# Performance work log

Measured on AMD Instinct MI355X. Metric: run time of the kernel, lower is better.

The kernel has to match this reference:

```python
import jax, jax.numpy as jnp
import numpy as np

B, N, E, H = 32, 512, 256, 8
HD = E // H
EPS = 1e-5

def setup_inputs() -> dict:
    key = jax.random.key(0)
    ks = jax.random.split(key, 10)
    x = jax.random.normal(ks[0], (B, N, E), dtype=jnp.float32)
    # boolean masks: True = masked out. Keep diagonal unmasked so no row is fully masked.
    pre = jax.random.bernoulli(ks[1], 0.1, (B, H, N, N))
    eye = jnp.eye(N, dtype=bool)
    pre_mask = jnp.where(eye[None, None, :, :], False, pre)
    post_attn_mask = jax.random.bernoulli(ks[2], 0.1, (B, N))
    s = 1.0 / np.sqrt(E)
    in_proj_w = jax.random.uniform(ks[3], (3 * E, E), jnp.float32, -s, s)
    in_proj_b = jnp.zeros((3 * E,), jnp.float32)
    out_w = jax.random.uniform(ks[4], (E, E), jnp.float32, -s, s)
    out_b = jnp.zeros((E,), jnp.float32)
    gamma = jnp.ones((E,), jnp.float32)
    beta = jnp.zeros((E,), jnp.float32)
    return {"x": x, "pre_mask": pre_mask, "post_attn_mask": post_attn_mask,
            "in_proj_w": in_proj_w, "in_proj_b": in_proj_b,
            "out_w": out_w, "out_b": out_b, "gamma": gamma, "beta": beta}

def reference(x, pre_mask, post_attn_mask, in_proj_w, in_proj_b, out_w, out_b, gamma, beta):
    b, n, e = x.shape
    # fused qkv projection (matches nn.MultiheadAttention in_proj)
    qkv = x @ in_proj_w.T + in_proj_b            # [B,N,3E]
    q, k, v = jnp.split(qkv, 3, axis=-1)
    def heads(t):
        return t.reshape(b, n, H, HD).transpose(0, 2, 1, 3)  # [B,H,N,HD]
    q, k, v = heads(q), heads(k), heads(v)
    scores = jnp.einsum('bhqd,bhkd->bhqk', q * (HD ** -0.5), k)  # [B,H,N,N]
    scores = jnp.where(pre_mask, -1e9, scores)
    w = jax.nn.softmax(scores, axis=-1)                          # [B,H,N,N]
    o = jnp.einsum('bhqk,bhkd->bhqd', w, v)                      # [B,H,N,HD]
    o = o.transpose(0, 2, 1, 3).reshape(b, n, e)
    o = o @ out_w.T + out_b
    # post-attention mask: zero outputs of unavailable agents
    o = jnp.where(post_attn_mask[:, :, None], 0.0, o)
    # residual + LayerNorm
    y = x + o
    mu = y.mean(axis=-1, keepdims=True)
    var = y.var(axis=-1, keepdims=True)
    out = (y - mu) * jax.lax.rsqrt(var + EPS) * gamma + beta
    # attn_weights averaged over heads (PyTorch default average_attn_weights=True)
    attn_weights = w.mean(axis=1)                                # [B,N,N]
    return (out, attn_weights)
```

## Files before the change

### kernel.cpp

```cpp
#include <hip/hip_runtime.h>

#define BB 32
#define NN 512
#define EE 256
#define HH 8
#define HDD 32

typedef __attribute__((ext_vector_type(4))) float f32x4;
typedef __attribute__((ext_vector_type(8))) short s16x8;
typedef unsigned short ushort_t;
typedef unsigned int uint_t;

__device__ __forceinline__ ushort_t f2bf(float f) {
  union { float f; uint_t u; } v; v.f = f;
  uint_t r = v.u + 0x7fffu + ((v.u >> 16) & 1u);
  return (ushort_t)(r >> 16);
}
__device__ __forceinline__ uint_t pk2(float a, float b) {
  return (uint_t)f2bf(a) | ((uint_t)f2bf(b) << 16);
}

__global__ __launch_bounds__(256) void cvt_bf16(
    const float* __restrict__ src, ushort_t* __restrict__ dst, int n4) {
  int i = blockIdx.x * 256 + threadIdx.x;
  if (i < n4) {
    float4 v = ((const float4*)src)[i];
    uint2 p; p.x = pk2(v.x, v.y); p.y = pk2(v.z, v.w);
    ((uint2*)dst)[i] = p;
  }
}

__global__ __launch_bounds__(256) void qkv_mfma(
    const ushort_t* __restrict__ xb, const ushort_t* __restrict__ wb,
    const float* __restrict__ bias,
    ushort_t* __restrict__ Q, ushort_t* __restrict__ K, ushort_t* __restrict__ Vt) {
  __shared__ ushort_t sA[128][40];
  __shared__ ushort_t sB[128][40];
  int t = threadIdx.x;
  int bj = blockIdx.x % 6, bm = blockIdx.x / 6;
  int m0 = bm * 128, j0 = bj * 128;
  int w4 = t >> 6, lane = t & 63, quad = lane >> 4, l16 = lane & 15;
  int wy = w4 >> 1, wx = w4 & 1;
  f32x4 acc[4][4];
  #pragma unroll
  for (int a = 0; a < 4; a++)
    #pragma unroll
    for (int b = 0; b < 4; b++) acc[a][b] = (f32x4){0.f, 0.f, 0.f, 0.f};
  int sr2 = t >> 2, sc2 = (t & 3) * 8;
  for (int kk = 0; kk < 256; kk += 32) {
    __syncthreads();
    #pragma unroll
    for (int p = 0; p < 2; p++) {
      int r = sr2 + 64 * p;
      *(s16x8*)&sA[r][sc2] = *(const s16x8*)&xb[(size_t)(m0 + r) * 256 + kk + sc2];
      *(s16x8*)&sB[r][sc2] = *(const s16x8*)&wb[(size_t)(j0 + r) * 256 + kk + sc2];
    }
    __syncthreads();
    s16x8 af[4], bf[4];
    #pragma unroll
    for (int mt = 0; mt < 4; mt++)
      af[mt] = *(const s16x8*)&sA[wy * 64 + mt * 16 + l16][quad * 8];
    #pragma unroll
    for (int jt = 0; jt < 4; jt++)
      bf[jt] = *(const s16x8*)&sB[wx * 64 + jt * 16 + l16][quad * 8];
    #pragma unroll
    for (int mt = 0; mt < 4; mt++)
      #pragma unroll
      for (int jt = 0; jt < 4; jt++)
        acc[mt][jt] = __builtin_amdgcn_mfma_f32_16x16x32_bf16(af[mt], bf[jt], acc[mt][jt], 0, 0, 0);
  }
  #pragma unroll
  for (int jt = 0; jt < 4; jt++) {
    int j = j0 + wx * 64 + jt * 16 + l16;
    int which = j >> 8, e0 = j & 255, h = e0 >> 5, d0 = e0 & 31;
    float b = bias[j];
    #pragma unroll
    for (int mt = 0; mt < 4; mt++) {
      #pragma unroll
      for (int r = 0; r < 4; r++) {
        int m = m0 + wy * 64 + mt * 16 + quad * 4 + r;
        int bi = m >> 9, n = m & 511;
        ushort_t val = f2bf(acc[mt][jt][r] + b);
        if (which == 2) {
          Vt[((size_t)(bi * 8 + h) * 32 + d0) * 512 + n] = val;
        } else {
          ushort_t* dst = (which == 0) ? Q : K;
          dst[((size_t)(bi * 8 + h) * 512 + n) * 32 + d0] = val;
        }
      }
    }
  }
}

__global__ __launch_bounds__(256) void attn_kernel(
    const ushort_t* __restrict__ Q, const ushort_t* __restrict__ K,
    const ushort_t* __restrict__ Vt, const int* __restrict__ pre_mask,
    ushort_t* __restrict__ O, float* __restrict__ attnw) {
  __shared__ ushort_t sQ[16 * 32];
  __shared__ ushort_t sP[16 * 520];
  __shared__ float sSum[4][16];
  __shared__ float sO[4][16 * 32];

  int t = threadIdx.x;
  int bb = blockIdx.x >> 5;
  int q0 = (blockIdx.x & 31) << 4;
  int w = t >> 6;
  int lane = t & 63;
  int quad = lane >> 4;
  int l16 = lane & 15;
  int kbase = w * 128;
  const float scale = 0.17677669529663687f;

  float wmean[4][8];
  #pragma unroll
  for (int i = 0; i < 4; i++)
    #pragma unroll
    for (int j = 0; j < 8; j++) wmean[i][j] = 0.f;

  for (int h = 0; h < 8; h++) {
    size_t base = ((size_t)(bb * 8 + h) * 512) * 32;
    const ushort_t* Kg = K + base;
    const ushort_t* Vg = Vt + base;
    const int* mbase = pre_mask + ((size_t)(bb * 8 + h) * 512 + q0) * 512;

    if (t < 64) {
      ((s16x8*)sQ)[t] = ((const s16x8*)(Q + base + (size_t)q0 * 32))[t];
    }
    __syncthreads();

    s16x8 afrag = *(const s16x8*)&sQ[l16 * 32 + quad * 8];
    float ev[8][4];
    #pragma unroll
    for (int t8 = 0; t8 < 8; t8++) {
      int n0 = kbase + t8 * 16;
      s16x8 bfrag = *(const s16x8*)&Kg[(size_t)(n0 + l16) * 32 + quad * 8];
      f32x4 acc = {0.f, 0.f, 0.f, 0.f};
      acc = __builtin_amdgcn_mfma_f32_16x16x32_bf16(afrag, bfrag, acc, 0, 0, 0);
      #pragma unroll
      for (int i = 0; i < 4; i++) {
        int msk = mbase[(quad * 4 + i) * 512 + n0 + l16];
        ev[t8][i] = msk ? 0.f : __expf(acc[i] * scale);
      }
    }
    float ps[4];
    #pragma unroll
    for (int i = 0; i < 4; i++) {
      float s = 0.f;
      #pragma unroll
      for (int t8 = 0; t8 < 8; t8++) s += ev[t8][i];
      s += __shfl_xor(s, 1, 64);
      s += __shfl_xor(s, 2, 64);
      s += __shfl_xor(s, 4, 64);
      s += __shfl_xor(s, 8, 64);
      ps[i] = s;
    }
    if (l16 == 0) {
      #pragma unroll
      for (int i = 0; i < 4; i++) sSum[w][quad * 4 + i] = ps[i];
    }
    #pragma unroll
    for (int t8 = 0; t8 < 8; t8++)
      #pragma unroll
      for (int i = 0; i < 4; i++)
        sP[(quad * 4 + i) * 520 + kbase + t8 * 16 + l16] = f2bf(ev[t8][i]);
    __syncthreads();

    float inv[4];
    #pragma unroll
    for (int i = 0; i < 4; i++) {
      int r = quad * 4 + i;
      inv[i] = 1.0f / (sSum[0][r] + sSum[1][r] + sSum[2][r] + sSum[3][r]);
    }
    #pragma unroll
    for (int t8 = 0; t8 < 8; t8++)
      #pragma unroll
      for (int i = 0; i < 4; i++)
        wmean[i][t8] += 0.125f * ev[t8][i] * inv[i];

    f32x4 oacc[2];
    oacc[0] = (f32x4){0.f, 0.f, 0.f, 0.f};
    oacc[1] = (f32x4){0.f, 0.f, 0.f, 0.f};
    #pragma unroll
    for (int ks = 0; ks < 4; ks++) {
      s16x8 pa = *(const s16x8*)&sP[l16 * 520 + kbase + ks * 32 + quad * 8];
      #pragma unroll
      for (int dt = 0; dt < 2; dt++) {
        s16x8 vb = *(const s16x8*)&Vg[(size_t)(dt * 16 + l16) * 512 + kbase + ks * 32 + quad * 8];
        oacc[dt] = __builtin_amdgcn_mfma_f32_16x16x32_bf16(pa, vb, oacc[dt], 0, 0, 0);
      }
    }
    #pragma unroll
    for (int dt = 0; dt < 2; dt++)
      #pragma unroll
      for (int i = 0; i < 4; i++)
        sO[w][(quad * 4 + i) * 32 + dt * 16 + l16] = oacc[dt][i];
    __syncthreads();

    {
      int r = t >> 4;
      int c = (t & 15) * 2;
      float s0 = sO[0][r * 32 + c] + sO[1][r * 32 + c] + sO[2][r * 32 + c] + sO[3][r * 32 + c];
      float s1 = sO[0][r * 32 + c + 1] + sO[1][r * 32 + c + 1] + sO[2][r * 32 + c + 1] + sO[3][r * 32 + c + 1];
      float invr = 1.0f / (sSum[0][r] + sSum[1][r] + sSum[2][r] + sSum[3][r]);
      uint_t pk = pk2(s0 * invr, s1 * invr);
      *(uint_t*)&O[((size_t)(bb * 512 + q0 + r) * 256) + h * 32 + c] = pk;
    }
  }

  float* arow = attnw + (size_t)(bb * 512 + q0) * 512;
  #pragma unroll
  for (int i = 0; i < 4; i++)
    #pragma unroll
    for (int t8 = 0; t8 < 8; t8++)
      arow[(quad * 4 + i) * 512 + kbase + t8 * 16 + l16] = wmean[i][t8];
}

__global__ __launch_bounds__(256) void proj_ln_mfma(
    const ushort_t* __restrict__ O, const float* __restrict__ x,
    const ushort_t* __restrict__ wb, const float* __restrict__ bias,
    const int* __restrict__ post_mask,
    const float* __restrict__ gamma, const float* __restrict__ beta,
    float* __restrict__ out) {
  __shared__ ushort_t sB[256][40];
  int t = threadIdx.x;
  int m0 = blockIdx.x * 64;
  int w4 = t >> 6, lane = t & 63, quad = lane >> 4, l16 = lane & 15;
  int mrow0 = m0 + w4 * 16;
  f32x4 acc[16];
  #pragma unroll
  for (int jt = 0; jt < 16; jt++) acc[jt] = (f32x4){0.f, 0.f, 0.f, 0.f};
  int sr2 = t >> 2, sc2 = (t & 3) * 8;
  for (int kk = 0; kk < 256; kk += 32) {
    __syncthreads();
    #pragma unroll
    for (int p = 0; p < 4; p++) {
      int r = sr2 + 64 * p;
      *(s16x8*)&sB[r][sc2] = *(const s16x8*)&wb[(size_t)r * 256 + kk + sc2];
    }
    __syncthreads();
    s16x8 af = *(const s16x8*)&O[(size_t)(mrow0 + l16) * 256 + kk + quad * 8];
    #pragma unroll
    for (int jt = 0; jt < 16; jt++) {
      s16x8 bf = *(const s16x8*)&sB[jt * 16 + l16][quad * 8];
      acc[jt] = __builtin_amdgcn_mfma_f32_16x16x32_bf16(af, bf, acc[jt], 0, 0, 0);
    }
  }
  #pragma unroll
  for (int i = 0; i < 4; i++) {
    int m = mrow0 + quad * 4 + i;
    int bi = m >> 9, n = m & 511;
    bool msk = post_mask[bi * 512 + n] != 0;
    float y[16];
    float s1 = 0.f, s2 = 0.f;
    #pragma unroll
    for (int jt = 0; jt < 16; jt++) {
      int j = jt * 16 + l16;
      float p = msk ? 0.f : (acc[jt][i] + bias[j]);
      float yy = x[(size_t)m * 256 + j] + p;
      y[jt] = yy; s1 += yy; s2 += yy * yy;
    }
    s1 += __shfl_xor(s1, 1, 64); s1 += __shfl_xor(s1, 2, 64);
    s1 += __shfl_xor(s1, 4, 64); s1 += __shfl_xor(s1, 8, 64);
    s2 += __shfl_xor(s2, 1, 64); s2 += __shfl_xor(s2, 2, 64);
    s2 += __shfl_xor(s2, 4, 64); s2 += __shfl_xor(s2, 8, 64);
    float mu = s1 * (1.0f / 256.0f);
    float var = s2 * (1.0f / 256.0f) - mu * mu;
    float rstd = rsqrtf(var + 1e-5f);
    #pragma unroll
    for (int jt = 0; jt < 16; jt++) {
      int j = jt * 16 + l16;
      out[(size_t)m * 256 + j] = (y[jt] - mu) * rstd * gamma[j] + beta[j];
    }
  }
}

extern "C" void kernel_launch(void* const* d_in, const int* in_sizes, int n_in,
                              void* d_out, int out_size, void* d_ws, size_t ws_size,
                              hipStream_t stream) {
  const float* x       = (const float*)d_in[0];
  const int*   pre_m   = (const int*)d_in[1];
  const int*   post_m  = (const int*)d_in[2];
  const float* in_w    = (const float*)d_in[3];
  const float* in_b    = (const float*)d_in[4];
  const float* out_w   = (const float*)d_in[5];
  const float* out_b   = (const float*)d_in[6];
  const float* gamma   = (const float*)d_in[7];
  const float* beta    = (const float*)d_in[8];
  float* out   = (float*)d_out;
  float* attnw = out + (size_t)BB * NN * EE;
  ushort_t* Q  = (ushort_t*)d_ws;
  ushort_t* K  = Q  + (size_t)BB * HH * NN * HDD;
  ushort_t* Vt = K  + (size_t)BB * HH * NN * HDD;
  ushort_t* O  = Vt + (size_t)BB * HH * NN * HDD;
  ushort_t* xb  = O  + (size_t)BB * NN * EE;
  ushort_t* wib = xb + (size_t)BB * NN * EE;
  ushort_t* wob = wib + (size_t)3 * EE * EE;

  cvt_bf16<<<dim3(4096), dim3(256), 0, stream>>>(x, xb, BB * NN * EE / 4);
  cvt_bf16<<<dim3(192), dim3(256), 0, stream>>>(in_w, wib, 3 * EE * EE / 4);
  cvt_bf16<<<dim3(64), dim3(256), 0, stream>>>(out_w, wob, EE * EE / 4);
  qkv_mfma<<<dim3(768), dim3(256), 0, stream>>>(xb, wib, in_b, Q, K, Vt);
  attn_kernel<<<dim3(1024), dim3(256), 0, stream>>>(Q, K, Vt, pre_m, O, attnw);
  proj_ln_mfma<<<dim3(256), dim3(256), 0, stream>>>(O, x, wob, out_b, post_m, gamma, beta, out);
}
```

Baseline: 486.4 us.

## Fuse output projection and LayerNorm into attention kernel; merge conversion launches

Folds the output projection GEMM, residual add, post-mask and LayerNorm into the attention kernel. Each block keeps its 16-row bf16 head outputs in shared memory and multiplies them by out_w read straight from global memory, so the O round trip through global memory and one launch go away. The three bf16 conversion kernels become a single launch. Softmax probabilities now go to per-wave shared tiles in place of a register array, the softmax-sum buffer is double-buffered by head parity, and the head average is read back from the bf16 tiles. That lowers register pressure but computes the averaged weights from rounded values, and each block re-reads the full out_w matrix.

Result: faster. 456.5 us (-6.2%).

```diff
diff --git a/kernel.cpp b/kernel.cpp
--- a/kernel.cpp
+++ b/kernel.cpp
@@ -19,15 +19,26 @@
 __device__ __forceinline__ uint_t pk2(float a, float b) {
   return (uint_t)f2bf(a) | ((uint_t)f2bf(b) << 16);
 }
-
-__global__ __launch_bounds__(256) void cvt_bf16(
-    const float* __restrict__ src, ushort_t* __restrict__ dst, int n4) {
+__device__ __forceinline__ float bf2f(ushort_t u) {
+  union { uint_t u; float f; } v; v.u = ((uint_t)u) << 16;
+  return v.f;
+}
+
+__global__ __launch_bounds__(256) void cvt_all(
+    const float* __restrict__ x, const float* __restrict__ w1, const float* __restrict__ w2,
+    ushort_t* __restrict__ xb, ushort_t* __restrict__ w1b, ushort_t* __restrict__ w2b) {
+  const int NX = BB * NN * EE / 4;
+  const int NW1 = 3 * EE * EE / 4;
+  const int NW2 = EE * EE / 4;
   int i = blockIdx.x * 256 + threadIdx.x;
-  if (i < n4) {
-    float4 v = ((const float4*)src)[i];
-    uint2 p; p.x = pk2(v.x, v.y); p.y = pk2(v.z, v.w);
-    ((uint2*)dst)[i] = p;
-  }
+  const float* src; ushort_t* dst; int j;
+  if (i < NX) { src = x; dst = xb; j = i; }
+  else if (i < NX + NW1) { src = w1; dst = w1b; j = i - NX; }
+  else if (i < NX + NW1 + NW2) { src = w2; dst = w2b; j = i - NX - NW1; }
+  else return;
+  float4 v = ((const float4*)src)[j];
+  uint2 p; p.x = pk2(v.x, v.y); p.y = pk2(v.z, v.w);
+  ((uint2*)dst)[j] = p;
 }
 
 __global__ __launch_bounds__(256) void qkv_mfma(
@@ -92,24 +103,27 @@
   }
 }
 
-__global__ __launch_bounds__(256) void attn_kernel(
+__global__ __launch_bounds__(256) void attn_fused(
     const ushort_t* __restrict__ Q, const ushort_t* __restrict__ K,
     const ushort_t* __restrict__ Vt, const int* __restrict__ pre_mask,
-    ushort_t* __restrict__ O, float* __restrict__ attnw) {
-  __shared__ ushort_t sQ[16 * 32];
-  __shared__ ushort_t sP[16 * 520];
-  __shared__ float sSum[4][16];
-  __shared__ float sO[4][16 * 32];
+    const ushort_t* __restrict__ wob, const float* __restrict__ x,
+    const float* __restrict__ out_b, const int* __restrict__ post_mask,
+    const float* __restrict__ gamma, const float* __restrict__ beta,
+    float* __restrict__ out, float* __restrict__ attnw) {
+  __shared__ ushort_t sP[4][16 * 132];
+  __shared__ float sSum[2][4][16];
+  __shared__ float sO[4][16 * 33];
+  __shared__ ushort_t sO16[16 * 260];
+  __shared__ float sRed1[16][4];
+  __shared__ float sRed2[16][4];
 
   int t = threadIdx.x;
   int bb = blockIdx.x >> 5;
   int q0 = (blockIdx.x & 31) << 4;
-  int w = t >> 6;
-  int lane = t & 63;
-  int quad = lane >> 4;
-  int l16 = lane & 15;
+  int w = t >> 6, lane = t & 63, quad = lane >> 4, l16 = lane & 15;
   int kbase = w * 128;
   const float scale = 0.17677669529663687f;
+  ushort_t* mysP = &sP[w][0];
 
   float wmean[4][8];
   #pragma unroll
@@ -119,73 +133,61 @@
 
   for (int h = 0; h < 8; h++) {
     size_t base = ((size_t)(bb * 8 + h) * 512) * 32;
-    const ushort_t* Kg = K + base;
-    const ushort_t* Vg = Vt + base;
     const int* mbase = pre_mask + ((size_t)(bb * 8 + h) * 512 + q0) * 512;
 
-    if (t < 64) {
-      ((s16x8*)sQ)[t] = ((const s16x8*)(Q + base + (size_t)q0 * 32))[t];
-    }
-    __syncthreads();
-
-    s16x8 afrag = *(const s16x8*)&sQ[l16 * 32 + quad * 8];
-    float ev[8][4];
+    s16x8 afrag = *(const s16x8*)&Q[base + (size_t)(q0 + l16) * 32 + quad * 8];
+
+    float psum[4] = {0.f, 0.f, 0.f, 0.f};
     #pragma unroll
     for (int t8 = 0; t8 < 8; t8++) {
       int n0 = kbase + t8 * 16;
-      s16x8 bfrag = *(const s16x8*)&Kg[(size_t)(n0 + l16) * 32 + quad * 8];
+      s16x8 bfrag = *(const s16x8*)&K[base + (size_t)(n0 + l16) * 32 + quad * 8];
       f32x4 acc = {0.f, 0.f, 0.f, 0.f};
       acc = __builtin_amdgcn_mfma_f32_16x16x32_bf16(afrag, bfrag, acc, 0, 0, 0);
       #pragma unroll
       for (int i = 0; i < 4; i++) {
         int msk = mbase[(quad * 4 + i) * 512 + n0 + l16];
-        ev[t8][i] = msk ? 0.f : __expf(acc[i] * scale);
+        float e = msk ? 0.f : __expf(acc[i] * scale);
+        mysP[(quad * 4 + i) * 132 + t8 * 16 + l16] = f2bf(e);
+        psum[i] += e;
       }
     }
-    float ps[4];
     #pragma unroll
     for (int i = 0; i < 4; i++) {
-      float s = 0.f;
-      #pragma unroll
-      for (int t8 = 0; t8 < 8; t8++) s += ev[t8][i];
+      float s = psum[i];
       s += __shfl_xor(s, 1, 64);
       s += __shfl_xor(s, 2, 64);
       s += __shfl_xor(s, 4, 64);
       s += __shfl_xor(s, 8, 64);
-      ps[i] = s;
+      psum[i] = s;
     }
     if (l16 == 0) {
       #pragma unroll
-      for (int i = 0; i < 4; i++) sSum[w][quad * 4 + i] = ps[i];
-    }
-    #pragma unroll
-    for (int t8 = 0; t8 < 8; t8++)
-      #pragma unroll
-      for (int i = 0; i < 4; i++)
-        sP[(quad * 4 + i) * 520 + kbase + t8 * 16 + l16] = f2bf(ev[t8][i]);
+      for (int i = 0; i < 4; i++) sSum[h & 1][w][quad * 4 + i] = psum[i];
+    }
     __syncthreads();
 
     float inv[4];
     #pragma unroll
     for (int i = 0; i < 4; i++) {
       int r = quad * 4 + i;
-      inv[i] = 1.0f / (sSum[0][r] + sSum[1][r] + sSum[2][r] + sSum[3][r]);
+      inv[i] = 0.125f / (sSum[h & 1][0][r] + sSum[h & 1][1][r] + sSum[h & 1][2][r] + sSum[h & 1][3][r]);
     }
     #pragma unroll
     for (int t8 = 0; t8 < 8; t8++)
       #pragma unroll
       for (int i = 0; i < 4; i++)
-        wmean[i][t8] += 0.125f * ev[t8][i] * inv[i];
+        wmean[i][t8] += inv[i] * bf2f(mysP[(quad * 4 + i) * 132 + t8 * 16 + l16]);
 
     f32x4 oacc[2];
     oacc[0] = (f32x4){0.f, 0.f, 0.f, 0.f};
     oacc[1] = (f32x4){0.f, 0.f, 0.f, 0.f};
     #pragma unroll
     for (int ks = 0; ks < 4; ks++) {
-      s16x8 pa = *(const s16x8*)&sP[l16 * 520 + kbase + ks * 32 + quad * 8];
+      s16x8 pa = *(const s16x8*)&mysP[l16 * 132 + ks * 32 + quad * 8];
       #pragma unroll
       for (int dt = 0; dt < 2; dt++) {
-        s16x8 vb = *(const s16x8*)&Vg[(size_t)(dt * 16 + l16) * 512 + kbase + ks * 32 + quad * 8];
+        s16x8 vb = *(const s16x8*)&Vt[base + (size_t)(dt * 16 + l16) * 512 + kbase + ks * 32 + quad * 8];
         oacc[dt] = __builtin_amdgcn_mfma_f32_16x16x32_bf16(pa, vb, oacc[dt], 0, 0, 0);
       }
     }
@@ -193,83 +195,83 @@
     for (int dt = 0; dt < 2; dt++)
       #pragma unroll
       for (int i = 0; i < 4; i++)
-        sO[w][(quad * 4 + i) * 32 + dt * 16 + l16] = oacc[dt][i];
+        sO[w][(quad * 4 + i) * 33 + dt * 16 + l16] = oacc[dt][i];
     __syncthreads();
 
     {
       int r = t >> 4;
       int c = (t & 15) * 2;
-      float s0 = sO[0][r * 32 + c] + sO[1][r * 32 + c] + sO[2][r * 32 + c] + sO[3][r * 32 + c];
-      float s1 = sO[0][r * 32 + c + 1] + sO[1][r * 32 + c + 1] + sO[2][r * 32 + c + 1] + sO[3][r * 32 + c + 1];
-      float invr = 1.0f / (sSum[0][r] + sSum[1][r] + sSum[2][r] + sSum[3][r]);
-      uint_t pk = pk2(s0 * invr, s1 * invr);
-      *(uint_t*)&O[((size_t)(bb * 512 + q0 + r) * 256) + h * 32 + c] = pk;
-    }
-  }
-
-  float* arow = attnw + (size_t)(bb * 512 + q0) * 512;
-  #pragma unroll
-  for (int i = 0; i < 4; i++)
-    #pragma unroll
-    for (int t8 = 0; t8 < 8; t8++)
-      arow[(quad * 4 + i) * 512 + kbase + t8 * 16 + l16] = wmean[i][t8];
-}
-
-__global__ __launch_bounds__(256) void proj_ln_mfma(
-    const ushort_t* __restrict__ O, const float* __restrict__ x,
-    const ushort_t* __restrict__ wb, const float* __restrict__ bias,
-    const int* __restrict__ post_mask,
-    const float* __restrict__ gamma, const float* __restrict__ beta,
-    float* __restrict__ out) {
-  __shared__ ushort_t sB[256][40];
-  int t = threadIdx.x;
-  int m0 = blockIdx.x * 64;
-  int w4 = t >> 6, lane = t & 63, quad = lane >> 4, l16 = lane & 15;
-  int mrow0 = m0 + w4 * 16;
-  f32x4 acc[16];
-  #pragma unroll
-  for (int jt = 0; jt < 16; jt++) acc[jt] = (f32x4){0.f, 0.f, 0.f, 0.f};
-  int sr2 = t >> 2, sc2 = (t & 3) * 8;
-  for (int kk = 0; kk < 256; kk += 32) {
-    __syncthreads();
-    #pragma unroll
-    for (int p = 0; p < 4; p++) {
-      int r = sr2 + 64 * p;
-      *(s16x8*)&sB[r][sc2] = *(const s16x8*)&wb[(size_t)r * 256 + kk + sc2];
-    }
-    __syncthreads();
-    s16x8 af = *(const s16x8*)&O[(size_t)(mrow0 + l16) * 256 + kk + quad * 8];
-    #pragma unroll
-    for (int jt = 0; jt < 16; jt++) {
-      s16x8 bf = *(const s16x8*)&sB[jt * 16 + l16][quad * 8];
-      acc[jt] = __builtin_amdgcn_mfma_f32_16x16x32_bf16(af, bf, acc[jt], 0, 0, 0);
-    }
-  }
+      float s0 = sO[0][r * 33 + c] + sO[1][r * 33 + c] + sO[2][r * 33 + c] + sO[3][r * 33 + c];
+      float s1 = sO[0][r * 33 + c + 1] + sO[1][r * 33 + c + 1] + sO[2][r * 33 + c + 1] + sO[3][r * 33 + c + 1];
+      float invr = 1.0f / (sSum[h & 1][0][r] + sSum[h & 1][1][r] + sSum[h & 1][2][r] + sSum[h & 1][3][r]);
+      *(uint_t*)&sO16[r * 260 + h * 32 + c] = pk2(s0 * invr, s1 * invr);
+    }
+  }
+
+  {
+    float* arow = attnw + (size_t)(bb * 512 + q0) * 512;
+    #pragma unroll
+    for (int i = 0; i < 4; i++)
+      #pragma unroll
+      for (int t8 = 0; t8 < 8; t8++)
+        arow[(quad * 4 + i) * 512 + kbase + t8 * 16 + l16] = wmean[i][t8];
+  }
+  __syncthreads();
+
+  int jr0 = w * 64;
+  f32x4 pacc[4];
+  #pragma unroll
+  for (int jt = 0; jt < 4; jt++) pacc[jt] = (f32x4){0.f, 0.f, 0.f, 0.f};
+  #pragma unroll
+  for (int kc = 0; kc < 8; kc++) {
+    s16x8 pa = *(const s16x8*)&sO16[l16 * 260 + kc * 32 + quad * 8];
+    #pragma unroll
+    for (int jt = 0; jt < 4; jt++) {
+      s16x8 bf = *(const s16x8*)&wob[(size_t)(jr0 + jt * 16 + l16) * 256 + kc * 32 + quad * 8];
+      pacc[jt] = __builtin_amdgcn_mfma_f32_16x16x32_bf16(pa, bf, pacc[jt], 0, 0, 0);
+    }
+  }
+
+  float g4[4], bt4[4], ob4[4];
+  #pragma unroll
+  for (int jt = 0; jt < 4; jt++) {
+    int j = jr0 + jt * 16 + l16;
+    g4[jt] = gamma[j]; bt4[jt] = beta[j]; ob4[jt] = out_b[j];
+  }
+  float yv[4][4];
   #pragma unroll
   for (int i = 0; i < 4; i++) {
-    int m = mrow0 + quad * 4 + i;
-    int bi = m >> 9, n = m & 511;
-    bool msk = post_mask[bi * 512 + n] != 0;
-    float y[16];
+    int r = quad * 4 + i;
+    int m = bb * 512 + q0 + r;
+    bool msk = post_mask[m] != 0;
     float s1 = 0.f, s2 = 0.f;
     #pragma unroll
-    for (int jt = 0; jt < 16; jt++) {
-      int j = jt * 16 + l16;
-      float p = msk ? 0.f : (acc[jt][i] + bias[j]);
+    for (int jt = 0; jt < 4; jt++) {
+      int j = jr0 + jt * 16 + l16;
+      float p = msk ? 0.f : (pacc[jt][i] + ob4[jt]);
       float yy = x[(size_t)m * 256 + j] + p;
-      y[jt] = yy; s1 += yy; s2 += yy * yy;
+      yv[i][jt] = yy; s1 += yy; s2 += yy * yy;
     }
     s1 += __shfl_xor(s1, 1, 64); s1 += __shfl_xor(s1, 2, 64);
     s1 += __shfl_xor(s1, 4, 64); s1 += __shfl_xor(s1, 8, 64);
     s2 += __shfl_xor(s2, 1, 64); s2 += __shfl_xor(s2, 2, 64);
     s2 += __shfl_xor(s2, 4, 64); s2 += __shfl_xor(s2, 8, 64);
-    float mu = s1 * (1.0f / 256.0f);
-    float var = s2 * (1.0f / 256.0f) - mu * mu;
+    if (l16 == 0) { sRed1[r][w] = s1; sRed2[r][w] = s2; }
+  }
+  __syncthreads();
+  #pragma unroll
+  for (int i = 0; i < 4; i++) {
+    int r = quad * 4 + i;
+    int m = bb * 512 + q0 + r;
+    float S1 = sRed1[r][0] + sRed1[r][1] + sRed1[r][2] + sRed1[r][3];
+    float S2 = sRed2[r][0] + sRed2[r][1] + sRed2[r][2] + sRed2[r][3];
+    float mu = S1 * (1.0f / 256.0f);
+    float var = S2 * (1.0f / 256.0f) - mu * mu;
     float rstd = rsqrtf(var + 1e-5f);
     #pragma unroll
-    for (int jt = 0; jt < 16; jt++) {
-      int j = jt * 16 + l16;
-      out[(size_t)m * 256 + j] = (y[jt] - mu) * rstd * gamma[j] + beta[j];
+    for (int jt = 0; jt < 4; jt++) {
+      int j = jr0 + jt * 16 + l16;
+      out[(size_t)m * 256 + j] = (yv[i][jt] - mu) * rstd * g4[jt] + bt4[jt];
     }
   }
 }
@@ -288,18 +290,16 @@
   const float* beta    = (const float*)d_in[8];
   float* out   = (float*)d_out;
   float* attnw = out + (size_t)BB * NN * EE;
-  ushort_t* Q  = (ushort_t*)d_ws;
-  ushort_t* K  = Q  + (size_t)BB * HH * NN * HDD;
-  ushort_t* Vt = K  + (size_t)BB * HH * NN * HDD;
-  ushort_t* O  = Vt + (size_t)BB * HH * NN * HDD;
-  ushort_t* xb  = O  + (size_t)BB * NN * EE;
+  ushort_t* Q   = (ushort_t*)d_ws;
+  ushort_t* K   = Q  + (size_t)BB * HH * NN * HDD;
+  ushort_t* Vt  = K  + (size_t)BB * HH * NN * HDD;
+  ushort_t* xb  = Vt + (size_t)BB * HH * NN * HDD;
   ushort_t* wib = xb + (size_t)BB * NN * EE;
   ushort_t* wob = wib + (size_t)3 * EE * EE;
 
-  cvt_bf16<<<dim3(4096), dim3(256), 0, stream>>>(x, xb, BB * NN * EE / 4);
-  cvt_bf16<<<dim3(192), dim3(256), 0, stream>>>(in_w, wib, 3 * EE * EE / 4);
-  cvt_bf16<<<dim3(64), dim3(256), 0, stream>>>(out_w, wob, EE * EE / 4);
+  const int NCVT = BB * NN * EE / 4 + 3 * EE * EE / 4 + EE * EE / 4;
+  cvt_all<<<dim3((NCVT + 255) / 256), dim3(256), 0, stream>>>(x, in_w, out_w, xb, wib, wob);
   qkv_mfma<<<dim3(768), dim3(256), 0, stream>>>(xb, wib, in_b, Q, K, Vt);
-  attn_kernel<<<dim3(1024), dim3(256), 0, stream>>>(Q, K, Vt, pre_m, O, attnw);
-  proj_ln_mfma<<<dim3(256), dim3(256), 0, stream>>>(O, x, wob, out_b, post_m, gamma, beta, out);
-}
+  attn_fused<<<dim3(1024), dim3(256), 0, stream>>>(Q, K, Vt, pre_m, wob, x, out_b, post_m,
+                                                   gamma, beta, out, attnw);
+}
```
